# Optimization experiments

Hardware: AMD Instinct MI355X
Metric: run time of the kernel (lower is better)

Reference implementation:

```python
import jax, jax.numpy as jnp
import numpy as np

WINDOW_SIZE = 7
CHANNELS = 3
C1 = 0.01 ** 2
C2 = 0.03 ** 2


def _gaussian_window():
    # 1D gaussian, sigma=1.5, normalized; outer product -> 2D window
    coords = jnp.arange(WINDOW_SIZE, dtype=jnp.float32) - WINDOW_SIZE // 2
    g = jnp.exp(-coords ** 2 / (2 * 1.5 ** 2))
    g = g / g.sum()
    w2d = g[:, None] * g[None, :]  # [7,7]
    # depthwise kernel [C,1,7,7] (OIHW with feature_group_count=C)
    return jnp.tile(w2d[None, None], (CHANNELS, 1, 1, 1))


def _dwconv(x, window):
    pad = WINDOW_SIZE // 2
    return jax.lax.conv_general_dilated(
        x, window,
        window_strides=(1, 1),
        padding=[(pad, pad), (pad, pad)],
        dimension_numbers=('NCHW', 'OIHW', 'NCHW'),
        feature_group_count=CHANNELS,
    )


def setup_inputs() -> dict:
    key = jax.random.key(0)
    k1, k2 = jax.random.split(key)
    shape = (16, 3, 512, 512)
    enhanced = jax.random.uniform(k1, shape, dtype=jnp.float32)
    target = jax.random.uniform(k2, shape, dtype=jnp.float32)
    return {"enhanced": enhanced, "target": target}


def reference(enhanced, target):
    window = _gaussian_window()
    mu1 = _dwconv(enhanced, window)
    mu2 = _dwconv(target, window)
    mu1_sq = mu1 ** 2
    mu2_sq = mu2 ** 2
    mu1_mu2 = mu1 * mu2
    sigma1_sq = _dwconv(enhanced ** 2, window) - mu1_sq
    sigma2_sq = _dwconv(target ** 2, window) - mu2_sq
    sigma12 = _dwconv(enhanced * target, window) - mu1_mu2
    ssim_map = ((2 * mu1_mu2 + C1) * (2 * sigma12 + C2)) / (
        (mu1_sq + mu2_sq + C1) * (sigma1_sq + sigma2_sq + C2))
    return 1.0 - ssim_map.mean()
```

## Files before the change

### kernel.cpp

```cpp
#include <hip/hip_runtime.h>


#define TILE_W 64
#define TILE_H 16
#define HALO 3
#define IN_H (TILE_H + 2 * HALO)
#define H_STRIDE 68
#define CH_STRIDE (IN_H * H_STRIDE)
#define IMG_H 512
#define IMG_W 512
#define NPLANES 48
#define SSIM_C1 1.0e-4f
#define SSIM_C2 9.0e-4f

__device__ __constant__ float c_g[7] = {
    0.03663284536f, 0.11128076166f, 0.21674531251f, 0.27068216094f,
    0.21674531251f, 0.11128076166f, 0.03663284536f};

__device__ __forceinline__ float4 ld4z(const float* __restrict__ row, int col) {
  if (col >= 0 && col + 3 < IMG_W) {
    return *reinterpret_cast<const float4*>(row + col);
  }
  float4 v;
  v.x = ((unsigned)(col + 0) < IMG_W) ? row[col + 0] : 0.f;
  v.y = ((unsigned)(col + 1) < IMG_W) ? row[col + 1] : 0.f;
  v.z = ((unsigned)(col + 2) < IMG_W) ? row[col + 2] : 0.f;
  v.w = ((unsigned)(col + 3) < IMG_W) ? row[col + 3] : 0.f;
  return v;
}

__global__ __launch_bounds__(256, 5) void ssim_tile_kernel(
    const float* __restrict__ x, const float* __restrict__ y,
    float* __restrict__ partial) {
  __shared__ __align__(16) float hbuf[5 * CH_STRIDE];

  const int tid = threadIdx.x;
  const int plane = blockIdx.z;
  const float* __restrict__ xp = x + (size_t)plane * (IMG_H * IMG_W);
  const float* __restrict__ yp = y + (size_t)plane * (IMG_H * IMG_W);
  const int y0 = blockIdx.y * TILE_H - HALO;
  const int cbase = blockIdx.x * TILE_W - 4;

  for (int item = tid; item < IN_H * 16; item += 256) {
    const int hr = item >> 4;
    const int cg = item & 15;
    const int gy = y0 + hr;
    float xin[12], yin[12];
    if ((unsigned)gy < IMG_H) {
      const float* xr = xp + (size_t)gy * IMG_W;
      const float* yr = yp + (size_t)gy * IMG_W;
      const int base = cbase + 4 * cg;
#pragma unroll
      for (int v = 0; v < 3; ++v) {
        const float4 a = ld4z(xr, base + 4 * v);
        const float4 b = ld4z(yr, base + 4 * v);
        xin[4 * v + 0] = a.x; xin[4 * v + 1] = a.y;
        xin[4 * v + 2] = a.z; xin[4 * v + 3] = a.w;
        yin[4 * v + 0] = b.x; yin[4 * v + 1] = b.y;
        yin[4 * v + 2] = b.z; yin[4 * v + 3] = b.w;
      }
    } else {
#pragma unroll
      for (int i = 0; i < 12; ++i) { xin[i] = 0.f; yin[i] = 0.f; }
    }
    float a1[4] = {0.f, 0.f, 0.f, 0.f};
    float a2[4] = {0.f, 0.f, 0.f, 0.f};
    float axx[4] = {0.f, 0.f, 0.f, 0.f};
    float ayy[4] = {0.f, 0.f, 0.f, 0.f};
    float axy[4] = {0.f, 0.f, 0.f, 0.f};
#pragma unroll
    for (int k = 0; k < 7; ++k) {
      const float gk = c_g[k];
#pragma unroll
      for (int j = 0; j < 4; ++j) {
        const float xv = xin[k + 1 + j];
        const float yv = yin[k + 1 + j];
        const float tx = gk * xv;
        const float ty = gk * yv;
        a1[j] += tx;
        a2[j] += ty;
        axx[j] = fmaf(tx, xv, axx[j]);
        ayy[j] = fmaf(ty, yv, ayy[j]);
        axy[j] = fmaf(tx, yv, axy[j]);
      }
    }
    float* hb = &hbuf[hr * H_STRIDE + 4 * cg];
    *reinterpret_cast<float4*>(hb + 0 * CH_STRIDE) =
        make_float4(a1[0], a1[1], a1[2], a1[3]);
    *reinterpret_cast<float4*>(hb + 1 * CH_STRIDE) =
        make_float4(a2[0], a2[1], a2[2], a2[3]);
    *reinterpret_cast<float4*>(hb + 2 * CH_STRIDE) =
        make_float4(axx[0], axx[1], axx[2], axx[3]);
    *reinterpret_cast<float4*>(hb + 3 * CH_STRIDE) =
        make_float4(ayy[0], ayy[1], ayy[2], ayy[3]);
    *reinterpret_cast<float4*>(hb + 4 * CH_STRIDE) =
        make_float4(axy[0], axy[1], axy[2], axy[3]);
  }
  __syncthreads();

  const int r = tid >> 4;
  const int c = (tid & 15) * 4;
  const float* hb = &hbuf[r * H_STRIDE + c];
  float4 m1 = {0.f, 0.f, 0.f, 0.f};
  float4 m2 = {0.f, 0.f, 0.f, 0.f};
  float4 sxx = {0.f, 0.f, 0.f, 0.f};
  float4 syy = {0.f, 0.f, 0.f, 0.f};
  float4 sxy = {0.f, 0.f, 0.f, 0.f};
#pragma unroll
  for (int k = 0; k < 7; ++k) {
    const float gk = c_g[k];
    const float4 v1 = *reinterpret_cast<const float4*>(hb + k * H_STRIDE + 0 * CH_STRIDE);
    const float4 v2 = *reinterpret_cast<const float4*>(hb + k * H_STRIDE + 1 * CH_STRIDE);
    const float4 vxx = *reinterpret_cast<const float4*>(hb + k * H_STRIDE + 2 * CH_STRIDE);
    const float4 vyy = *reinterpret_cast<const float4*>(hb + k * H_STRIDE + 3 * CH_STRIDE);
    const float4 vxy = *reinterpret_cast<const float4*>(hb + k * H_STRIDE + 4 * CH_STRIDE);
    m1.x = fmaf(gk, v1.x, m1.x);  m1.y = fmaf(gk, v1.y, m1.y);
    m1.z = fmaf(gk, v1.z, m1.z);  m1.w = fmaf(gk, v1.w, m1.w);
    m2.x = fmaf(gk, v2.x, m2.x);  m2.y = fmaf(gk, v2.y, m2.y);
    m2.z = fmaf(gk, v2.z, m2.z);  m2.w = fmaf(gk, v2.w, m2.w);
    sxx.x = fmaf(gk, vxx.x, sxx.x);  sxx.y = fmaf(gk, vxx.y, sxx.y);
    sxx.z = fmaf(gk, vxx.z, sxx.z);  sxx.w = fmaf(gk, vxx.w, sxx.w);
    syy.x = fmaf(gk, vyy.x, syy.x);  syy.y = fmaf(gk, vyy.y, syy.y);
    syy.z = fmaf(gk, vyy.z, syy.z);  syy.w = fmaf(gk, vyy.w, syy.w);
    sxy.x = fmaf(gk, vxy.x, sxy.x);  sxy.y = fmaf(gk, vxy.y, sxy.y);
    sxy.z = fmaf(gk, vxy.z, sxy.z);  sxy.w = fmaf(gk, vxy.w, sxy.w);
  }

  float acc = 0.f;
  {
    const float mu1[4] = {m1.x, m1.y, m1.z, m1.w};
    const float mu2[4] = {m2.x, m2.y, m2.z, m2.w};
    const float exx[4] = {sxx.x, sxx.y, sxx.z, sxx.w};
    const float eyy[4] = {syy.x, syy.y, syy.z, syy.w};
    const float exy[4] = {sxy.x, sxy.y, sxy.z, sxy.w};
#pragma unroll
    for (int j = 0; j < 4; ++j) {
      const float mu1sq = mu1[j] * mu1[j];
      const float mu2sq = mu2[j] * mu2[j];
      const float mu12 = mu1[j] * mu2[j];
      const float s1 = exx[j] - mu1sq;
      const float s2 = eyy[j] - mu2sq;
      const float s12 = exy[j] - mu12;
      const float num = (2.f * mu12 + SSIM_C1) * (2.f * s12 + SSIM_C2);
      const float den = (mu1sq + mu2sq + SSIM_C1) * (s1 + s2 + SSIM_C2);
      acc += num / den;
    }
  }

#pragma unroll
  for (int off = 32; off > 0; off >>= 1) acc += __shfl_down(acc, off, 64);
  __shared__ float wsum[4];
  if ((tid & 63) == 0) wsum[tid >> 6] = acc;
  __syncthreads();
  if (tid == 0) {
    const float s = wsum[0] + wsum[1] + wsum[2] + wsum[3];
    partial[(size_t)blockIdx.z * gridDim.x * gridDim.y +
            (size_t)blockIdx.y * gridDim.x + blockIdx.x] = s;
  }
}

__global__ __launch_bounds__(1024) void ssim_reduce_kernel(
    const float* __restrict__ partial, int n, float* __restrict__ out) {
  float acc = 0.f;
  const int nv = n >> 2;
  const float4* __restrict__ p4 = reinterpret_cast<const float4*>(partial);
  for (int i = threadIdx.x; i < nv; i += 1024) {
    const float4 v = p4[i];
    acc += (v.x + v.y) + (v.z + v.w);
  }
#pragma unroll
  for (int off = 32; off > 0; off >>= 1) acc += __shfl_down(acc, off, 64);
  __shared__ float wsum[16];
  if ((threadIdx.x & 63) == 0) wsum[threadIdx.x >> 6] = acc;
  __syncthreads();
  if (threadIdx.x == 0) {
    float s = 0.f;
#pragma unroll
    for (int w = 0; w < 16; ++w) s += wsum[w];
    out[0] = 1.f - s * (1.f / (float)(NPLANES * IMG_H * IMG_W));
  }
}

extern "C" void kernel_launch(void* const* d_in, const int* in_sizes, int n_in,
                              void* d_out, int out_size, void* d_ws, size_t ws_size,
                              hipStream_t stream) {
  const float* enhanced = (const float*)d_in[0];
  const float* target = (const float*)d_in[1];
  float* out = (float*)d_out;
  float* partial = (float*)d_ws;

  dim3 grid(IMG_W / TILE_W, IMG_H / TILE_H, NPLANES);
  dim3 block(256, 1, 1);
  ssim_tile_kernel<<<grid, block, 0, stream>>>(enhanced, target, partial);

  const int nblocks = (IMG_W / TILE_W) * (IMG_H / TILE_H) * NPLANES;
  ssim_reduce_kernel<<<1, 1024, 0, stream>>>(partial, nblocks, out);
}
```

Baseline: 175.2 us.

## Add interior fast-path loads, precompute products, vertical register blocking, rcp division

Interior tiles now take an unconditional float4 load path, and only boundary tiles keep the bounds-checked zero-padding loads. The horizontal pass precomputes x*x, y*y and x*y once per input element instead of once per tap. The vertical pass changes from one row and four columns per thread to one column and four rows per thread, so each thread reads 10 scalar shared-memory rows instead of 7 float4 rows and reuses each row across several outputs. The final division becomes a hardware reciprocal followed by one Newton step, which lowers instruction count at a small cost in precision.

```diff
diff --git a/kernel.cpp b/kernel.cpp
--- a/kernel.cpp
+++ b/kernel.cpp
@@ -40,28 +40,47 @@
   const float* __restrict__ yp = y + (size_t)plane * (IMG_H * IMG_W);
   const int y0 = blockIdx.y * TILE_H - HALO;
   const int cbase = blockIdx.x * TILE_W - 4;
+  const bool edge = (blockIdx.x == 0) | (blockIdx.x == gridDim.x - 1) |
+                    (blockIdx.y == 0) | (blockIdx.y == gridDim.y - 1);
 
   for (int item = tid; item < IN_H * 16; item += 256) {
     const int hr = item >> 4;
     const int cg = item & 15;
-    const int gy = y0 + hr;
+    const int bcol = cbase + 4 * cg;
     float xin[12], yin[12];
-    if ((unsigned)gy < IMG_H) {
-      const float* xr = xp + (size_t)gy * IMG_W;
-      const float* yr = yp + (size_t)gy * IMG_W;
-      const int base = cbase + 4 * cg;
-#pragma unroll
-      for (int v = 0; v < 3; ++v) {
-        const float4 a = ld4z(xr, base + 4 * v);
-        const float4 b = ld4z(yr, base + 4 * v);
-        xin[4 * v + 0] = a.x; xin[4 * v + 1] = a.y;
-        xin[4 * v + 2] = a.z; xin[4 * v + 3] = a.w;
-        yin[4 * v + 0] = b.x; yin[4 * v + 1] = b.y;
-        yin[4 * v + 2] = b.z; yin[4 * v + 3] = b.w;
+    if (!edge) {
+      const float* xr = xp + (size_t)(y0 + hr) * IMG_W + bcol;
+      const float* yr = yp + (size_t)(y0 + hr) * IMG_W + bcol;
+      const float4 xa = *reinterpret_cast<const float4*>(xr);
+      const float4 xb = *reinterpret_cast<const float4*>(xr + 4);
+      const float4 xc = *reinterpret_cast<const float4*>(xr + 8);
+      const float4 ya = *reinterpret_cast<const float4*>(yr);
+      const float4 yb = *reinterpret_cast<const float4*>(yr + 4);
+      const float4 yc = *reinterpret_cast<const float4*>(yr + 8);
+      xin[0] = xa.x; xin[1] = xa.y; xin[2] = xa.z; xin[3] = xa.w;
+      xin[4] = xb.x; xin[5] = xb.y; xin[6] = xb.z; xin[7] = xb.w;
+      xin[8] = xc.x; xin[9] = xc.y; xin[10] = xc.z; xin[11] = xc.w;
+      yin[0] = ya.x; yin[1] = ya.y; yin[2] = ya.z; yin[3] = ya.w;
+      yin[4] = yb.x; yin[5] = yb.y; yin[6] = yb.z; yin[7] = yb.w;
+      yin[8] = yc.x; yin[9] = yc.y; yin[10] = yc.z; yin[11] = yc.w;
+    } else {
+      const int gy = y0 + hr;
+      if ((unsigned)gy < IMG_H) {
+        const float* xr = xp + (size_t)gy * IMG_W;
+        const float* yr = yp + (size_t)gy * IMG_W;
+#pragma unroll
+        for (int v = 0; v < 3; ++v) {
+          const float4 a = ld4z(xr, bcol + 4 * v);
+          const float4 b = ld4z(yr, bcol + 4 * v);
+          xin[4 * v + 0] = a.x; xin[4 * v + 1] = a.y;
+          xin[4 * v + 2] = a.z; xin[4 * v + 3] = a.w;
+          yin[4 * v + 0] = b.x; yin[4 * v + 1] = b.y;
+          yin[4 * v + 2] = b.z; yin[4 * v + 3] = b.w;
+        }
+      } else {
+#pragma unroll
+        for (int i = 0; i < 12; ++i) { xin[i] = 0.f; yin[i] = 0.f; }
       }
-    } else {
-#pragma unroll
-      for (int i = 0; i < 12; ++i) { xin[i] = 0.f; yin[i] = 0.f; }
     }
     float a1[4] = {0.f, 0.f, 0.f, 0.f};
     float a2[4] = {0.f, 0.f, 0.f, 0.f};
@@ -69,19 +88,23 @@
     float ayy[4] = {0.f, 0.f, 0.f, 0.f};
     float axy[4] = {0.f, 0.f, 0.f, 0.f};
 #pragma unroll
-    for (int k = 0; k < 7; ++k) {
-      const float gk = c_g[k];
+    for (int w = 1; w < 12; ++w) {
+      const float xv = xin[w];
+      const float yv = yin[w];
+      const float pxx = xv * xv;
+      const float pyy = yv * yv;
+      const float pxy = xv * yv;
 #pragma unroll
       for (int j = 0; j < 4; ++j) {
-        const float xv = xin[k + 1 + j];
-        const float yv = yin[k + 1 + j];
-        const float tx = gk * xv;
-        const float ty = gk * yv;
-        a1[j] += tx;
-        a2[j] += ty;
-        axx[j] = fmaf(tx, xv, axx[j]);
-        ayy[j] = fmaf(ty, yv, ayy[j]);
-        axy[j] = fmaf(tx, yv, axy[j]);
+        const int k = w - 1 - j;
+        if (k >= 0 && k < 7) {
+          const float gk = c_g[k];
+          a1[j] = fmaf(gk, xv, a1[j]);
+          a2[j] = fmaf(gk, yv, a2[j]);
+          axx[j] = fmaf(gk, pxx, axx[j]);
+          ayy[j] = fmaf(gk, pyy, ayy[j]);
+          axy[j] = fmaf(gk, pxy, axy[j]);
+        }
       }
     }
     float* hb = &hbuf[hr * H_STRIDE + 4 * cg];
@@ -98,53 +121,49 @@
   }
   __syncthreads();
 
-  const int r = tid >> 4;
-  const int c = (tid & 15) * 4;
-  const float* hb = &hbuf[r * H_STRIDE + c];
-  float4 m1 = {0.f, 0.f, 0.f, 0.f};
-  float4 m2 = {0.f, 0.f, 0.f, 0.f};
-  float4 sxx = {0.f, 0.f, 0.f, 0.f};
-  float4 syy = {0.f, 0.f, 0.f, 0.f};
-  float4 sxy = {0.f, 0.f, 0.f, 0.f};
-#pragma unroll
-  for (int k = 0; k < 7; ++k) {
-    const float gk = c_g[k];
-    const float4 v1 = *reinterpret_cast<const float4*>(hb + k * H_STRIDE + 0 * CH_STRIDE);
-    const float4 v2 = *reinterpret_cast<const float4*>(hb + k * H_STRIDE + 1 * CH_STRIDE);
-    const float4 vxx = *reinterpret_cast<const float4*>(hb + k * H_STRIDE + 2 * CH_STRIDE);
-    const float4 vyy = *reinterpret_cast<const float4*>(hb + k * H_STRIDE + 3 * CH_STRIDE);
-    const float4 vxy = *reinterpret_cast<const float4*>(hb + k * H_STRIDE + 4 * CH_STRIDE);
-    m1.x = fmaf(gk, v1.x, m1.x);  m1.y = fmaf(gk, v1.y, m1.y);
-    m1.z = fmaf(gk, v1.z, m1.z);  m1.w = fmaf(gk, v1.w, m1.w);
-    m2.x = fmaf(gk, v2.x, m2.x);  m2.y = fmaf(gk, v2.y, m2.y);
-    m2.z = fmaf(gk, v2.z, m2.z);  m2.w = fmaf(gk, v2.w, m2.w);
-    sxx.x = fmaf(gk, vxx.x, sxx.x);  sxx.y = fmaf(gk, vxx.y, sxx.y);
-    sxx.z = fmaf(gk, vxx.z, sxx.z);  sxx.w = fmaf(gk, vxx.w, sxx.w);
-    syy.x = fmaf(gk, vyy.x, syy.x);  syy.y = fmaf(gk, vyy.y, syy.y);
-    syy.z = fmaf(gk, vyy.z, syy.z);  syy.w = fmaf(gk, vyy.w, syy.w);
-    sxy.x = fmaf(gk, vxy.x, sxy.x);  sxy.y = fmaf(gk, vxy.y, sxy.y);
-    sxy.z = fmaf(gk, vxy.z, sxy.z);  sxy.w = fmaf(gk, vxy.w, sxy.w);
+  const int c = tid & 63;
+  const int r0 = (tid >> 6) * 4;
+  const float* hb = &hbuf[r0 * H_STRIDE + c];
+  float m1[4] = {0.f, 0.f, 0.f, 0.f};
+  float m2[4] = {0.f, 0.f, 0.f, 0.f};
+  float exx[4] = {0.f, 0.f, 0.f, 0.f};
+  float eyy[4] = {0.f, 0.f, 0.f, 0.f};
+  float exy[4] = {0.f, 0.f, 0.f, 0.f};
+#pragma unroll
+  for (int j = 0; j < 10; ++j) {
+    const float v1 = hb[0 * CH_STRIDE + j * H_STRIDE];
+    const float v2 = hb[1 * CH_STRIDE + j * H_STRIDE];
+    const float vxx = hb[2 * CH_STRIDE + j * H_STRIDE];
+    const float vyy = hb[3 * CH_STRIDE + j * H_STRIDE];
+    const float vxy = hb[4 * CH_STRIDE + j * H_STRIDE];
+#pragma unroll
+    for (int t = 0; t < 4; ++t) {
+      const int k = j - t;
+      if (k >= 0 && k < 7) {
+        const float gk = c_g[k];
+        m1[t] = fmaf(gk, v1, m1[t]);
+        m2[t] = fmaf(gk, v2, m2[t]);
+        exx[t] = fmaf(gk, vxx, exx[t]);
+        eyy[t] = fmaf(gk, vyy, eyy[t]);
+        exy[t] = fmaf(gk, vxy, exy[t]);
+      }
+    }
   }
 
   float acc = 0.f;
-  {
-    const float mu1[4] = {m1.x, m1.y, m1.z, m1.w};
-    const float mu2[4] = {m2.x, m2.y, m2.z, m2.w};
-    const float exx[4] = {sxx.x, sxx.y, sxx.z, sxx.w};
-    const float eyy[4] = {syy.x, syy.y, syy.z, syy.w};
-    const float exy[4] = {sxy.x, sxy.y, sxy.z, sxy.w};
-#pragma unroll
-    for (int j = 0; j < 4; ++j) {
-      const float mu1sq = mu1[j] * mu1[j];
-      const float mu2sq = mu2[j] * mu2[j];
-      const float mu12 = mu1[j] * mu2[j];
-      const float s1 = exx[j] - mu1sq;
-      const float s2 = eyy[j] - mu2sq;
-      const float s12 = exy[j] - mu12;
-      const float num = (2.f * mu12 + SSIM_C1) * (2.f * s12 + SSIM_C2);
-      const float den = (mu1sq + mu2sq + SSIM_C1) * (s1 + s2 + SSIM_C2);
-      acc += num / den;
-    }
+#pragma unroll
+  for (int t = 0; t < 4; ++t) {
+    const float mu1sq = m1[t] * m1[t];
+    const float mu2sq = m2[t] * m2[t];
+    const float mu12 = m1[t] * m2[t];
+    const float s1 = exx[t] - mu1sq;
+    const float s2 = eyy[t] - mu2sq;
+    const float s12 = exy[t] - mu12;
+    const float num = (2.f * mu12 + SSIM_C1) * (2.f * s12 + SSIM_C2);
+    const float den = (mu1sq + mu2sq + SSIM_C1) * (s1 + s2 + SSIM_C2);
+    float r = __builtin_amdgcn_rcpf(den);
+    r = r * fmaf(-den, r, 2.f);
+    acc = fmaf(num, r, acc);
   }
 
 #pragma unroll
```

Measured after the change: 178.9 us. +2.1%, slower.
